# Optimization experiments

Hardware: AMD Instinct MI355X
Metric: run time of the kernel (lower is better)

The kernel has to match this reference:

```python
import jax, jax.numpy as jnp
import numpy as np

H = 8      # hidden_size
IN = 14    # input_size
B = 4096   # batch
T = 512    # seq_len
BN_EPS = 1e-5


def setup_inputs() -> dict:
    key = jax.random.key(0)
    ks = jax.random.split(key, 16)
    s = lambda k, shape, scale=0.25: jax.random.normal(k, shape, jnp.float32) * scale
    return {
        "x": jax.random.normal(ks[0], (B, T, IN), jnp.float32),
        # layer 1 LSTM params (PyTorch gate order: i, f, g, o)
        "Wih1": s(ks[1], (4 * H, IN)), "Whh1": s(ks[2], (4 * H, H)),
        "bih1": s(ks[3], (4 * H,)), "bhh1": s(ks[4], (4 * H,)),
        # layer 2 LSTM params
        "Wih2": s(ks[5], (4 * H, H)), "Whh2": s(ks[6], (4 * H, H)),
        "bih2": s(ks[7], (4 * H,)), "bhh2": s(ks[8], (4 * H,)),
        # BatchNorm1d(H) params + running stats (eval mode)
        "bn_gamma": jnp.ones((H,), jnp.float32), "bn_beta": jnp.zeros((H,), jnp.float32),
        "bn_mean": s(ks[9], (H,), 0.01), "bn_var": jnp.ones((H,), jnp.float32),
        # MLP head
        "w1": s(ks[10], (4, H)), "b1": s(ks[11], (4,)),
        "w2": s(ks[12], (1, 4)), "b2": s(ks[13], (1,)),
    }


def _cell(gates, c):
    # gates: [B, 4H] pre-activation, PyTorch order i, f, g, o
    i, f, g, o = jnp.split(gates, 4, axis=-1)
    c_new = jax.nn.sigmoid(f) * c + jax.nn.sigmoid(i) * jnp.tanh(g)
    h_new = jax.nn.sigmoid(o) * jnp.tanh(c_new)
    return h_new, c_new


def _lstm_last(x, Wih1, Whh1, bih1, bhh1, Wih2, Whh2, bih2, bhh2):
    # x: [B, T, IN] -> returns last hidden state of layer 2: [B, H]
    xt = jnp.swapaxes(x, 0, 1)  # [T, B, IN]
    # precompute input projections for layer 1 in one big GEMM
    xp1 = jnp.einsum('tbf,gf->tbg', xt, Wih1) + (bih1 + bhh1)  # [T, B, 4H]
    b2sum = bih2 + bhh2
    Bn = x.shape[0]
    z = jnp.zeros((Bn, H), x.dtype)
    init = (z, z, z, z)  # h1, c1, h2, c2

    def step(carry, xp):
        h1, c1, h2, c2 = carry
        h1, c1 = _cell(xp + h1 @ Whh1.T, c1)
        h2, c2 = _cell(h1 @ Wih2.T + h2 @ Whh2.T + b2sum, c2)
        return (h1, c1, h2, c2), None

    (h1, c1, h2, c2), _ = jax.lax.scan(step, init, xp1)
    return h2


def reference(x, Wih1, Whh1, bih1, bhh1, Wih2, Whh2, bih2, bhh2,
              bn_gamma, bn_beta, bn_mean, bn_var, w1, b1, w2, b2):
    last = _lstm_last(x, Wih1, Whh1, bih1, bhh1, Wih2, Whh2, bih2, bhh2)  # [B, H]
    # BatchNorm1d in eval mode (running stats); dropout is identity in eval
    normed = bn_gamma * (last - bn_mean) / jnp.sqrt(bn_var + BN_EPS) + bn_beta
    h = jax.nn.relu(normed @ w1.T + b1)  # [B, 4]
    out = h @ w2.T + b2                  # [B, 1]
    return out.squeeze(-1)               # [B]
```

## Files before the change

kernel.cpp:

```cpp
#include <hip/hip_runtime.h>

#define T_SEQ 512
#define INPUT 14
#define HID 8
#define TC 16
#define NCHUNK (T_SEQ / TC)
#define BN_EPS 1e-5f

typedef float v2f __attribute__((ext_vector_type(2)));

__device__ __forceinline__ float fast_exp2(float x) { return __builtin_amdgcn_exp2f(x); }
__device__ __forceinline__ float fast_rcp(float x)  { return __builtin_amdgcn_rcpf(x); }

__device__ __forceinline__ v2f pk_fma(v2f a, v2f b, v2f c) {
    v2f d;
    asm("v_pk_fma_f32 %0, %1, %2, %3" : "=v"(d) : "v"(a), "v"(b), "v"(c));
    return d;
}
__device__ __forceinline__ v2f pk_mul(v2f a, v2f b) {
    v2f d;
    asm("v_pk_mul_f32 %0, %1, %2" : "=v"(d) : "v"(a), "v"(b));
    return d;
}
__device__ __forceinline__ v2f pk_add(v2f a, v2f b) {
    v2f d;
    asm("v_pk_add_f32 %0, %1, %2" : "=v"(d) : "v"(a), "v"(b));
    return d;
}

template <int IMM>
__device__ __forceinline__ float swz(float v) {
    return __int_as_float(__builtin_amdgcn_ds_swizzle(__float_as_int(v), IMM));
}

#define DPP_BC0  0x00
#define DPP_BC1  0x55
#define DPP_BC2  0xAA
#define DPP_BC3  0xFF
#define DPP_XOR8 0x128
template <int CTRL>
__device__ __forceinline__ float dpp(float v) {
    return __int_as_float(__builtin_amdgcn_update_dpp(
        0, __float_as_int(v), CTRL, 0xF, 0xF, true));
}

__device__ __forceinline__ void butterfly8v(float h, v2f (&hx)[4]) {
    float x4  = swz<0x101F>(h);
    float x16 = swz<0x401F>(h);
    float x20 = swz<0x501F>(h);
    hx[0].x = h;
    hx[0].y = x4;
    hx[1].x = dpp<DPP_XOR8>(h);
    hx[1].y = dpp<DPP_XOR8>(x4);
    hx[2].x = x16;
    hx[2].y = x20;
    hx[3].x = dpp<DPP_XOR8>(x16);
    hx[3].y = dpp<DPP_XOR8>(x20);
}

__global__ __launch_bounds__(256, 2)
void lstm_forex_kernel(const float* __restrict__ x,
                       const float* __restrict__ Wih1, const float* __restrict__ Whh1,
                       const float* __restrict__ bih1, const float* __restrict__ bhh1,
                       const float* __restrict__ Wih2, const float* __restrict__ Whh2,
                       const float* __restrict__ bih2, const float* __restrict__ bhh2,
                       const float* __restrict__ bn_gamma, const float* __restrict__ bn_beta,
                       const float* __restrict__ bn_mean, const float* __restrict__ bn_var,
                       const float* __restrict__ w1p, const float* __restrict__ b1p,
                       const float* __restrict__ w2p, const float* __restrict__ b2p,
                       float* __restrict__ out)
{
    __shared__ float xbuf[4][2][TC][16];

    const int tid  = threadIdx.x;
    const int wave = tid >> 6;
    const int lane = tid & 63;
    const int grp  = lane >> 5;
    const int l5   = lane & 31;
    const int u    = (l5 >> 2) & 7;
    const int type = l5 & 3;
    const int row  = type * 8 + u;

    const int b = blockIdx.x * 8 + wave * 2 + grp;

    const float gateScale = (type == 2) ? -2.885390082f : -1.4426950408f;
    const float actMul    = (type == 2) ? -5.770780164f : 1.f;
    const float actAdd    = (type == 2) ?  2.885390082f : 0.f;

    v2f wi1p[7], wh1v[4], wi2v[4], wh2v[4];
#pragma unroll
    for (int k = 0; k < 7; ++k) {
        wi1p[k].x = Wih1[row * INPUT + 2 * k]     * gateScale;
        wi1p[k].y = Wih1[row * INPUT + 2 * k + 1] * gateScale;
    }
#pragma unroll
    for (int p = 0; p < 4; ++p) {
        int j0 = u ^ (2 * p), j1 = u ^ (2 * p + 1);
        wh1v[p].x = Whh1[row * HID + j0] * gateScale;
        wh1v[p].y = Whh1[row * HID + j1] * gateScale;
        wi2v[p].x = Wih2[row * HID + j0] * gateScale;
        wi2v[p].y = Wih2[row * HID + j1] * gateScale;
        wh2v[p].x = Whh2[row * HID + j0] * gateScale;
        wh2v[p].y = Whh2[row * HID + j1] * gateScale;
    }
    const float bsum1s = (bih1[row] + bhh1[row]) * gateScale;
    const float bsum2s = (bih2[row] + bhh2[row]) * gateScale;
    const v2f   bias1  = { bsum1s, 0.f };
    const v2f   bias2  = { bsum2s, 0.f };

    const float* gptr[7];
    int loff[7];
#pragma unroll
    for (int it = 0; it < 7; ++it) {
        int d   = it * 64 + lane;
        int es  = d / 224;
        int idx = d - es * 224;
        int tr  = idx / 14;
        int k   = idx - tr * 14;
        int bb  = blockIdx.x * 8 + wave * 2 + es;
        gptr[it] = x + (size_t)bb * (T_SEQ * INPUT) + idx;
        loff[it] = es * (TC * 16) + tr * 16 + k;
    }

    v2f hx1[4], hx2[4];
    float c1 = 0.f, c2 = 0.f;
#pragma unroll
    for (int p = 0; p < 4; ++p) { hx1[p] = (v2f){0.f, 0.f}; hx2[p] = (v2f){0.f, 0.f}; }

    float st[7];
#pragma unroll
    for (int it = 0; it < 7; ++it) { st[it] = *gptr[it]; gptr[it] += TC * INPUT; }

    float (*xw)[TC][16] = xbuf[wave];

    for (int c = 0; c < NCHUNK; ++c) {
#pragma unroll
        for (int it = 0; it < 7; ++it) ((float*)xw)[loff[it]] = st[it];
        if (c + 1 < NCHUNK) {
#pragma unroll
            for (int it = 0; it < 7; ++it) { st[it] = *gptr[it]; gptr[it] += TC * INPUT; }
        }
        __builtin_amdgcn_wave_barrier();

#pragma unroll
        for (int t = 0; t < TC; ++t) {
            const float* xrow = &xw[grp][t][0];
            float4 xa = *(const float4*)(xrow + 0);
            float4 xb = *(const float4*)(xrow + 4);
            float4 xc = *(const float4*)(xrow + 8);
            float2 xd = *(const float2*)(xrow + 12);

            v2f ax0 = pk_fma((v2f){xa.x, xa.y}, wi1p[0], bias1);
            v2f ax1 = pk_mul((v2f){xa.z, xa.w}, wi1p[1]);
            ax0 = pk_fma((v2f){xb.x, xb.y}, wi1p[2], ax0);
            ax1 = pk_fma((v2f){xb.z, xb.w}, wi1p[3], ax1);
            ax0 = pk_fma((v2f){xc.x, xc.y}, wi1p[4], ax0);
            ax1 = pk_fma((v2f){xc.z, xc.w}, wi1p[5], ax1);
            ax0 = pk_fma((v2f){xd.x, xd.y}, wi1p[6], ax0);

            v2f qA = pk_fma(hx2[0], wh2v[0], bias2);
            v2f qB = pk_mul(hx2[1], wh2v[1]);
            qA = pk_fma(hx2[2], wh2v[2], qA);
            qB = pk_fma(hx2[3], wh2v[3], qB);

            v2f sA = pk_fma(hx1[0], wh1v[0], ax0);
            v2f sB = pk_fma(hx1[1], wh1v[1], ax1);
            sA = pk_fma(hx1[2], wh1v[2], sA);
            sB = pk_fma(hx1[3], wh1v[3], sB);
            v2f sC = pk_add(sA, sB);
            float acc = sC.x + sC.y;

            float v0 = fmaf(fast_rcp(1.f + fast_exp2(acc)), actMul, actAdd);
            float vi = dpp<DPP_BC0>(v0);
            float vf = dpp<DPP_BC1>(v0);
            float vg = dpp<DPP_BC2>(v0);
            float vo = dpp<DPP_BC3>(v0);
            c1 = fmaf(vf, c1, vi * vg);
            float th1 = fmaf(fast_rcp(1.f + fast_exp2(c1)), 2.f, -1.f);
            float h1u = vo * th1;
            butterfly8v(h1u, hx1);

            v2f pA = pk_fma(hx1[0], wi2v[0], qA);
            v2f pB = pk_fma(hx1[1], wi2v[1], qB);
            pA = pk_fma(hx1[2], wi2v[2], pA);
            pB = pk_fma(hx1[3], wi2v[3], pB);
            v2f pC = pk_add(pA, pB);
            float acc2 = pC.x + pC.y;

            float u0 = fmaf(fast_rcp(1.f + fast_exp2(acc2)), actMul, actAdd);
            float ui = dpp<DPP_BC0>(u0);
            float uf = dpp<DPP_BC1>(u0);
            float ug = dpp<DPP_BC2>(u0);
            float uo = dpp<DPP_BC3>(u0);
            c2 = fmaf(uf, c2, ui * ug);
            float th2 = fmaf(fast_rcp(1.f + fast_exp2(c2)), 2.f, -1.f);
            float h2u = uo * th2;
            butterfly8v(h2u, hx2);
        }
    }

    if (l5 == 0) {
        float h2v[HID];
#pragma unroll
        for (int j = 0; j < HID; ++j) h2v[j] = (j & 1) ? hx2[j >> 1].y : hx2[j >> 1].x;
        float nd[HID];
#pragma unroll
        for (int j = 0; j < HID; ++j) {
            float inv = 1.f / sqrtf(bn_var[j] + BN_EPS);
            nd[j] = bn_gamma[j] * (h2v[j] - bn_mean[j]) * inv + bn_beta[j];
        }
        float acc = b2p[0];
#pragma unroll
        for (int m = 0; m < 4; ++m) {
            float s = b1p[m];
#pragma unroll
            for (int j = 0; j < HID; ++j) s = fmaf(nd[j], w1p[m * HID + j], s);
            s = fmaxf(s, 0.f);
            acc = fmaf(s, w2p[m], acc);
        }
        out[b] = acc;
    }
}

extern "C" void kernel_launch(void* const* d_in, const int* in_sizes, int n_in,
                              void* d_out, int out_size, void* d_ws, size_t ws_size,
                              hipStream_t stream) {
    const float* x        = (const float*)d_in[0];
    const float* Wih1     = (const float*)d_in[1];
    const float* Whh1     = (const float*)d_in[2];
    const float* bih1     = (const float*)d_in[3];
    const float* bhh1     = (const float*)d_in[4];
    const float* Wih2     = (const float*)d_in[5];
    const float* Whh2     = (const float*)d_in[6];
    const float* bih2     = (const float*)d_in[7];
    const float* bhh2     = (const float*)d_in[8];
    const float* bn_gamma = (const float*)d_in[9];
    const float* bn_beta  = (const float*)d_in[10];
    const float* bn_mean  = (const float*)d_in[11];
    const float* bn_var   = (const float*)d_in[12];
    const float* w1p      = (const float*)d_in[13];
    const float* b1p      = (const float*)d_in[14];
    const float* w2p      = (const float*)d_in[15];
    const float* b2p      = (const float*)d_in[16];
    float* out = (float*)d_out;

    const int B = in_sizes[0] / (T_SEQ * INPUT);
    dim3 grid(B / 8), block(256);
    hipLaunchKernelGGL(lstm_forex_kernel, grid, block, 0, stream,
                       x, Wih1, Whh1, bih1, bhh1, Wih2, Whh2, bih2, bhh2,
                       bn_gamma, bn_beta, bn_mean, bn_var, w1p, b1p, w2p, b2p, out);
}
```

Before: 318.7 us.

## Remap gate lanes so hidden broadcast uses quad-perm DPP and permlane16 swap

Reassigns the lane-to-(unit,gate) mapping so the four gates of a unit sit 4 lanes apart and the eight hidden units span quad positions plus a 16-lane half. Gate gathering now uses row-rotate DPP with selects, and the hidden-state broadcast uses quad-perm DPP plus a permlane16 swap (or a swizzle fallback) in place of ds_swizzle-heavy butterflies. The aim is to cut LDS-routed swizzle latency on the serial recurrence path, at the cost of extra select instructions. The x-row loads from LDS are also rewritten as float2 vector loads.

```diff
diff --git a/kernel.cpp b/kernel.cpp
--- a/kernel.cpp
+++ b/kernel.cpp
@@ -33,29 +33,30 @@
     return __int_as_float(__builtin_amdgcn_ds_swizzle(__float_as_int(v), IMM));
 }
 
-#define DPP_BC0  0x00
-#define DPP_BC1  0x55
-#define DPP_BC2  0xAA
-#define DPP_BC3  0xFF
-#define DPP_XOR8 0x128
+#define DPP_QP1   0xB1
+#define DPP_QP2   0x4E
+#define DPP_QP3   0x1B
+#define DPP_ROR4  0x124
+#define DPP_ROR8  0x128
+#define DPP_ROR12 0x12C
 template <int CTRL>
 __device__ __forceinline__ float dpp(float v) {
     return __int_as_float(__builtin_amdgcn_update_dpp(
         0, __float_as_int(v), CTRL, 0xF, 0xF, true));
 }
-
-__device__ __forceinline__ void butterfly8v(float h, v2f (&hx)[4]) {
-    float x4  = swz<0x101F>(h);
-    float x16 = swz<0x401F>(h);
-    float x20 = swz<0x501F>(h);
-    hx[0].x = h;
-    hx[0].y = x4;
-    hx[1].x = dpp<DPP_XOR8>(h);
-    hx[1].y = dpp<DPP_XOR8>(x4);
-    hx[2].x = x16;
-    hx[2].y = x20;
-    hx[3].x = dpp<DPP_XOR8>(x16);
-    hx[3].y = dpp<DPP_XOR8>(x20);
+template <int CTRL>
+__device__ __forceinline__ int dpp_i(int v) {
+    return __builtin_amdgcn_update_dpp(0, v, CTRL, 0xF, 0xF, true);
+}
+
+__device__ __forceinline__ float xor16v(float h) {
+#if __has_builtin(__builtin_amdgcn_permlane16_swap)
+    unsigned hb = __float_as_uint(h);
+    auto r = __builtin_amdgcn_permlane16_swap(hb, hb, false, false);
+    return __uint_as_float(r[0] ^ r[1] ^ hb);
+#else
+    return swz<0x401F>(h);
+#endif
 }
 
 __global__ __launch_bounds__(256, 2)
@@ -77,11 +78,16 @@
     const int lane = tid & 63;
     const int grp  = lane >> 5;
     const int l5   = lane & 31;
-    const int u    = (l5 >> 2) & 7;
-    const int type = l5 & 3;
+    const int u    = (l5 & 3) | ((l5 >> 2) & 4);
+    const int type = (l5 >> 2) & 3;
     const int row  = type * 8 + u;
+    const bool tb0 = (type & 1) != 0;
+    const bool tb1 = (type & 2) != 0;
 
     const int b = blockIdx.x * 8 + wave * 2 + grp;
+
+    const int got   = dpp_i<DPP_ROR4>(l5);
+    const bool dplus = (got == ((l5 & 16) | ((l5 + 4) & 15)));
 
     const float gateScale = (type == 2) ? -2.885390082f : -1.4426950408f;
     const float actMul    = (type == 2) ? -5.770780164f : 1.f;
@@ -95,7 +101,7 @@
     }
 #pragma unroll
     for (int p = 0; p < 4; ++p) {
-        int j0 = u ^ (2 * p), j1 = u ^ (2 * p + 1);
+        int j0 = u ^ (2 * p), j1 = j0 ^ 1;
         wh1v[p].x = Whh1[row * HID + j0] * gateScale;
         wh1v[p].y = Whh1[row * HID + j1] * gateScale;
         wi2v[p].x = Wih2[row * HID + j0] * gateScale;
@@ -144,19 +150,17 @@
 
 #pragma unroll
         for (int t = 0; t < TC; ++t) {
-            const float* xrow = &xw[grp][t][0];
-            float4 xa = *(const float4*)(xrow + 0);
-            float4 xb = *(const float4*)(xrow + 4);
-            float4 xc = *(const float4*)(xrow + 8);
-            float2 xd = *(const float2*)(xrow + 12);
-
-            v2f ax0 = pk_fma((v2f){xa.x, xa.y}, wi1p[0], bias1);
-            v2f ax1 = pk_mul((v2f){xa.z, xa.w}, wi1p[1]);
-            ax0 = pk_fma((v2f){xb.x, xb.y}, wi1p[2], ax0);
-            ax1 = pk_fma((v2f){xb.z, xb.w}, wi1p[3], ax1);
-            ax0 = pk_fma((v2f){xc.x, xc.y}, wi1p[4], ax0);
-            ax1 = pk_fma((v2f){xc.z, xc.w}, wi1p[5], ax1);
-            ax0 = pk_fma((v2f){xd.x, xd.y}, wi1p[6], ax0);
+            const v2f* xv = (const v2f*)&xw[grp][t][0];
+            v2f x0 = xv[0], x1 = xv[1], x2 = xv[2], x3 = xv[3];
+            v2f x4 = xv[4], x5 = xv[5], x6 = xv[6];
+
+            v2f ax0 = pk_fma(x0, wi1p[0], bias1);
+            v2f ax1 = pk_mul(x1, wi1p[1]);
+            ax0 = pk_fma(x2, wi1p[2], ax0);
+            ax1 = pk_fma(x3, wi1p[3], ax1);
+            ax0 = pk_fma(x4, wi1p[4], ax0);
+            ax1 = pk_fma(x5, wi1p[5], ax1);
+            ax0 = pk_fma(x6, wi1p[6], ax0);
 
             v2f qA = pk_fma(hx2[0], wh2v[0], bias2);
             v2f qB = pk_mul(hx2[1], wh2v[1]);
@@ -171,14 +175,32 @@
             float acc = sC.x + sC.y;
 
             float v0 = fmaf(fast_rcp(1.f + fast_exp2(acc)), actMul, actAdd);
-            float vi = dpp<DPP_BC0>(v0);
-            float vf = dpp<DPP_BC1>(v0);
-            float vg = dpp<DPP_BC2>(v0);
-            float vo = dpp<DPP_BC3>(v0);
-            c1 = fmaf(vf, c1, vi * vg);
+            float r1 = dpp<DPP_ROR4>(v0);
+            float r2 = dpp<DPP_ROR8>(v0);
+            float r3 = dpp<DPP_ROR12>(v0);
+            float va = dplus ? r1 : r3;
+            float vb = dplus ? r3 : r1;
+            float m02 = v0 * r2;
+            float m13 = va * vb;
+            float P = tb0 ? m13 : m02;
+            float sF1 = tb0 ? v0 : va;
+            float sF2 = tb0 ? r2 : vb;
+            float F = tb1 ? sF2 : sF1;
+            float O = tb1 ? sF1 : sF2;
+            c1 = fmaf(F, c1, P);
             float th1 = fmaf(fast_rcp(1.f + fast_exp2(c1)), 2.f, -1.f);
-            float h1u = vo * th1;
-            butterfly8v(h1u, hx1);
+            float h1u = O * th1;
+            butterfly: ;
+            {
+                float y1 = dpp<DPP_QP1>(h1u);
+                float y2 = dpp<DPP_QP2>(h1u);
+                float y3 = dpp<DPP_QP3>(h1u);
+                float y16 = xor16v(h1u);
+                hx1[0].x = h1u; hx1[0].y = y1;
+                hx1[1].x = y2;  hx1[1].y = y3;
+                hx1[2].x = y16; hx1[2].y = dpp<DPP_QP1>(y16);
+                hx1[3].x = dpp<DPP_QP2>(y16); hx1[3].y = dpp<DPP_QP3>(y16);
+            }
 
             v2f pA = pk_fma(hx1[0], wi2v[0], qA);
             v2f pB = pk_fma(hx1[1], wi2v[1], qB);
@@ -187,22 +209,41 @@
             v2f pC = pk_add(pA, pB);
             float acc2 = pC.x + pC.y;
 
-            float u0 = fmaf(fast_rcp(1.f + fast_exp2(acc2)), actMul, actAdd);
-            float ui = dpp<DPP_BC0>(u0);
-            float uf = dpp<DPP_BC1>(u0);
-            float ug = dpp<DPP_BC2>(u0);
-            float uo = dpp<DPP_BC3>(u0);
-            c2 = fmaf(uf, c2, ui * ug);
+            float w0 = fmaf(fast_rcp(1.f + fast_exp2(acc2)), actMul, actAdd);
+            float z1 = dpp<DPP_ROR4>(w0);
+            float z2 = dpp<DPP_ROR8>(w0);
+            float z3 = dpp<DPP_ROR12>(w0);
+            float wa = dplus ? z1 : z3;
+            float wb = dplus ? z3 : z1;
+            float n02 = w0 * z2;
+            float n13 = wa * wb;
+            float P2 = tb0 ? n13 : n02;
+            float tF1 = tb0 ? w0 : wa;
+            float tF2 = tb0 ? z2 : wb;
+            float F2 = tb1 ? tF2 : tF1;
+            float O2 = tb1 ? tF1 : tF2;
+            c2 = fmaf(F2, c2, P2);
             float th2 = fmaf(fast_rcp(1.f + fast_exp2(c2)), 2.f, -1.f);
-            float h2u = uo * th2;
-            butterfly8v(h2u, hx2);
+            float h2u = O2 * th2;
+            {
+                float y1 = dpp<DPP_QP1>(h2u);
+                float y2 = dpp<DPP_QP2>(h2u);
+                float y3 = dpp<DPP_QP3>(h2u);
+                float y16 = xor16v(h2u);
+                hx2[0].x = h2u; hx2[0].y = y1;
+                hx2[1].x = y2;  hx2[1].y = y3;
+                hx2[2].x = y16; hx2[2].y = dpp<DPP_QP1>(y16);
+                hx2[3].x = dpp<DPP_QP2>(y16); hx2[3].y = dpp<DPP_QP3>(y16);
+            }
         }
     }
 
     if (l5 == 0) {
         float h2v[HID];
-#pragma unroll
-        for (int j = 0; j < HID; ++j) h2v[j] = (j & 1) ? hx2[j >> 1].y : hx2[j >> 1].x;
+        h2v[0] = hx2[0].x; h2v[1] = hx2[0].y;
+        h2v[2] = hx2[1].x; h2v[3] = hx2[1].y;
+        h2v[4] = hx2[2].x; h2v[5] = hx2[2].y;
+        h2v[6] = hx2[3].x; h2v[7] = hx2[3].y;
         float nd[HID];
 #pragma unroll
         for (int j = 0; j < HID; ++j) {
```

New measurement: 357.1 us. +12.0%, slower.
